# Optimization experiments

Hardware: AMD Instinct MI355X
Metric: run time of the kernel (lower is better)

## Reference

```python
import jax, jax.numpy as jnp
import numpy as np

SIZE = 128
B, S = 32, 8192


def setup_inputs() -> dict:
    key = jax.random.key(0)
    kx, = jax.random.split(key, 1)
    x = jax.random.normal(kx, (B, S, SIZE), dtype=jnp.float32)
    return {
        "x": x,
        # DyT params
        "alpha": jnp.ones((1,), jnp.float32) * 0.5,
        "dyt_weight": jnp.ones((SIZE,), jnp.float32),
        "dyt_bias": jnp.zeros((SIZE,), jnp.float32),
        # FourierForwardNetwork params
        "a_real": jnp.ones((SIZE,), jnp.float32),
        "a_imag": jnp.zeros((SIZE,), jnp.float32),
        "b_real": jnp.ones((SIZE,), jnp.float32),
        "b_imag": jnp.zeros((SIZE,), jnp.float32),
        "ffn_bias": jnp.zeros((SIZE,), jnp.float32),
    }


def reference(x, alpha, dyt_weight, dyt_bias, a_real, a_imag, b_real, b_imag, ffn_bias):
    # DyT: tanh(alpha * x) * weight + bias
    h = jnp.tanh(alpha * x) * dyt_weight + dyt_bias  # [B, S, SIZE]
    # FourierForwardNetwork. NOTE: in the original torch code the first
    # spectral branch (multiply by a, ifft, +bias, gelu) is DEAD CODE --
    # its result is overwritten by `X = torch.fft.fft(x + 0j)`. The actual
    # output is ifft(fft(h) * b).real, reproduced faithfully here.
    b = b_real + 1j * b_imag  # [SIZE] complex
    X = jnp.fft.fft(h.astype(jnp.complex64), axis=-1)  # [B, S, SIZE] complex64
    y = jnp.fft.ifft(X * b, axis=-1).real.astype(x.dtype)
    # Residual connection of FourierFFNBlock
    return y + x
```

## Files before the change

### kernel.cpp

```cpp
#include <hip/hip_runtime.h>

#define SIZE 128
#define ROWS 32
#define TPB 8
#define PITCH 136

typedef short short8 __attribute__((ext_vector_type(8)));
typedef float f32x4 __attribute__((ext_vector_type(4)));

__device__ __forceinline__ unsigned short f2bf(float f) {
    unsigned int u = __float_as_uint(f);
    unsigned int r = u + 0x7FFFu + ((u >> 16) & 1u);
    return (unsigned short)(r >> 16);
}

__global__ void build_gt(const float* __restrict__ br, const float* __restrict__ bi,
                         const float* __restrict__ w, const float* __restrict__ bias,
                         unsigned short* __restrict__ Gt, float* __restrict__ C0) {
    __shared__ float gr[SIZE];
    const int t = threadIdx.x;
    float acc = 0.0f;
    for (int j = 0; j < SIZE; ++j) {
        int p = (j * t) & 127;
        float a = (float)p * (1.0f / 64.0f);
        acc += br[j] * cospif(a) - bi[j] * sinpif(a);
    }
    gr[t] = acc * (1.0f / 128.0f);
    __syncthreads();
    float c0 = 0.0f;
    for (int k = 0; k < SIZE; ++k) {
        const float g = gr[(t - k) & 127];
        c0 += bias[k] * g;
        Gt[t * SIZE + k] = f2bf(w[k] * g);
    }
    C0[t] = c0;
}

__global__ __launch_bounds__(256, 4) void fourier_main(
    const float* __restrict__ x, const float* __restrict__ alpha_p,
    const unsigned short* __restrict__ Gt, const float* __restrict__ C0,
    float* __restrict__ out) {
    __shared__ unsigned short hA[2][ROWS * PITCH];

    const int tid = threadIdx.x;
    const int lane = tid & 63;
    const int wv = tid >> 6;
    const int lrow = lane & 15;
    const int slot = lane >> 4;
    const int colb = wv * 32;

    const float a2l = 2.0f * 1.44269504f * alpha_p[0];

    short8 gf[2][4];
    float4 c0v[2];
#pragma unroll
    for (int nt = 0; nt < 2; ++nt) {
        const int c = colb + nt * 16 + lrow;
#pragma unroll
        for (int kt = 0; kt < 4; ++kt)
            gf[nt][kt] = *reinterpret_cast<const short8*>(
                &Gt[c * SIZE + kt * 32 + slot * 8]);
        c0v[nt] = *reinterpret_cast<const float4*>(&C0[colb + nt * 16 + slot * 4]);
    }

    const unsigned blockBase = (unsigned)blockIdx.x * (TPB * ROWS * SIZE);
    const int srow = tid >> 5;
    const int scol = (tid & 31) * 4;

    auto stage = [&](int t, float4 (&xn)[4]) __attribute__((always_inline)) {
        const float* src = x + blockBase + (unsigned)t * (ROWS * SIZE);
#pragma unroll
        for (int i = 0; i < 4; ++i)
            xn[i] = *reinterpret_cast<const float4*>(&src[i * 1024 + tid * 4]);
    };
    auto hwrite = [&](int buf, const float4 (&xn)[4]) __attribute__((always_inline)) {
#pragma unroll
        for (int i = 0; i < 4; ++i) {
            ushort4 hq;
            float e;
            e = __builtin_amdgcn_exp2f(a2l * xn[i].x);
            hq.x = f2bf(fmaf(-2.0f, __builtin_amdgcn_rcpf(1.0f + e), 1.0f));
            e = __builtin_amdgcn_exp2f(a2l * xn[i].y);
            hq.y = f2bf(fmaf(-2.0f, __builtin_amdgcn_rcpf(1.0f + e), 1.0f));
            e = __builtin_amdgcn_exp2f(a2l * xn[i].z);
            hq.z = f2bf(fmaf(-2.0f, __builtin_amdgcn_rcpf(1.0f + e), 1.0f));
            e = __builtin_amdgcn_exp2f(a2l * xn[i].w);
            hq.w = f2bf(fmaf(-2.0f, __builtin_amdgcn_rcpf(1.0f + e), 1.0f));
            *reinterpret_cast<ushort4*>(&hA[buf][(i * 8 + srow) * PITCH + scol]) = hq;
        }
    };
    auto compute = [&](int t) __attribute__((always_inline)) {
        const unsigned tb = blockBase + (unsigned)t * (ROWS * SIZE);
        const unsigned short* hb = &hA[t & 1][0];
#pragma unroll
        for (int mt = 0; mt < 2; ++mt) {
            const int r = mt * 16 + lrow;
            short8 hf[4];
#pragma unroll
            for (int kt = 0; kt < 4; ++kt)
                hf[kt] = *reinterpret_cast<const short8*>(
                    &hb[r * PITCH + kt * 32 + slot * 8]);
#pragma unroll
            for (int nt = 0; nt < 2; ++nt) {
                f32x4 a = {0.f, 0.f, 0.f, 0.f};
#pragma unroll
                for (int kt = 0; kt < 4; ++kt)
                    a = __builtin_amdgcn_mfma_f32_16x16x32_bf16(gf[nt][kt], hf[kt],
                                                                a, 0, 0, 0);
                const unsigned off =
                    tb + (unsigned)r * SIZE + (unsigned)(colb + nt * 16 + slot * 4);
                const float4 xa = *reinterpret_cast<const float4*>(&x[off]);
                float4 o;
                o.x = a[0] + c0v[nt].x + xa.x;
                o.y = a[1] + c0v[nt].y + xa.y;
                o.z = a[2] + c0v[nt].z + xa.z;
                o.w = a[3] + c0v[nt].w + xa.w;
                *reinterpret_cast<float4*>(&out[off]) = o;
            }
        }
    };

    float4 xn[4];
    stage(0, xn);
    hwrite(0, xn);
    asm volatile("s_waitcnt lgkmcnt(0)\n\ts_barrier" ::: "memory");

#pragma unroll
    for (int t = 0; t < TPB; ++t) {
        if (t + 1 < TPB) stage(t + 1, xn);
        compute(t);
        if (t + 1 < TPB) {
            hwrite((t + 1) & 1, xn);
            asm volatile("s_waitcnt lgkmcnt(0)\n\ts_barrier" ::: "memory");
        }
    }
}

extern "C" void kernel_launch(void* const* d_in, const int* in_sizes, int n_in,
                              void* d_out, int out_size, void* d_ws, size_t ws_size,
                              hipStream_t stream) {
    const float* x = (const float*)d_in[0];
    const float* alpha = (const float*)d_in[1];
    const float* dyt_w = (const float*)d_in[2];
    const float* dyt_b = (const float*)d_in[3];
    const float* b_real = (const float*)d_in[6];
    const float* b_imag = (const float*)d_in[7];
    float* out = (float*)d_out;

    unsigned short* Gt = (unsigned short*)d_ws;
    float* C0 = (float*)((char*)d_ws + SIZE * SIZE * 2);

    build_gt<<<1, 128, 0, stream>>>(b_real, b_imag, dyt_w, dyt_b, Gt, C0);

    const int rows = out_size / SIZE;
    const int nblocks = rows / (ROWS * TPB);
    fourier_main<<<nblocks, 256, 0, stream>>>(x, alpha, Gt, C0, out);
}
```

Before: 76.88 us.

## Stage x in MFMA-output layout and reuse registers for residual

Each thread now loads x in the same fragment layout the MFMA output uses, so the staged float4 registers serve both the tanh/LDS write and the residual add. This removes the second global read of x per tile. It also double-buffers the register staging so loads for tile t+2 are issued while tile t computes. The cost is more live registers per thread and a less contiguous LDS write pattern, which may cause bank conflicts or reduce occupancy under the launch bounds.

```diff
diff --git a/kernel.cpp b/kernel.cpp
--- a/kernel.cpp
+++ b/kernel.cpp
@@ -64,42 +64,56 @@
     }
 
     const unsigned blockBase = (unsigned)blockIdx.x * (TPB * ROWS * SIZE);
-    const int srow = tid >> 5;
-    const int scol = (tid & 31) * 4;
+    unsigned soff[2][2];
+#pragma unroll
+    for (int mt = 0; mt < 2; ++mt)
+#pragma unroll
+        for (int nt = 0; nt < 2; ++nt)
+            soff[mt][nt] =
+                (unsigned)((mt * 16 + lrow) * SIZE + colb + nt * 16 + slot * 4);
 
-    auto stage = [&](int t, float4 (&xn)[4]) __attribute__((always_inline)) {
-        const float* src = x + blockBase + (unsigned)t * (ROWS * SIZE);
+    auto stage = [&](int t, float4 (&xs)[2][2]) __attribute__((always_inline)) {
+        const unsigned tb = blockBase + (unsigned)t * (ROWS * SIZE);
 #pragma unroll
-        for (int i = 0; i < 4; ++i)
-            xn[i] = *reinterpret_cast<const float4*>(&src[i * 1024 + tid * 4]);
+        for (int mt = 0; mt < 2; ++mt)
+#pragma unroll
+            for (int nt = 0; nt < 2; ++nt)
+                xs[mt][nt] =
+                    *reinterpret_cast<const float4*>(&x[tb + soff[mt][nt]]);
     };
-    auto hwrite = [&](int buf, const float4 (&xn)[4]) __attribute__((always_inline)) {
+    auto hwrite = [&](int buf, const float4 (&xs)[2][2])
+        __attribute__((always_inline)) {
 #pragma unroll
-        for (int i = 0; i < 4; ++i) {
-            ushort4 hq;
-            float e;
-            e = __builtin_amdgcn_exp2f(a2l * xn[i].x);
-            hq.x = f2bf(fmaf(-2.0f, __builtin_amdgcn_rcpf(1.0f + e), 1.0f));
-            e = __builtin_amdgcn_exp2f(a2l * xn[i].y);
-            hq.y = f2bf(fmaf(-2.0f, __builtin_amdgcn_rcpf(1.0f + e), 1.0f));
-            e = __builtin_amdgcn_exp2f(a2l * xn[i].z);
-            hq.z = f2bf(fmaf(-2.0f, __builtin_amdgcn_rcpf(1.0f + e), 1.0f));
-            e = __builtin_amdgcn_exp2f(a2l * xn[i].w);
-            hq.w = f2bf(fmaf(-2.0f, __builtin_amdgcn_rcpf(1.0f + e), 1.0f));
-            *reinterpret_cast<ushort4*>(&hA[buf][(i * 8 + srow) * PITCH + scol]) = hq;
-        }
+        for (int mt = 0; mt < 2; ++mt)
+#pragma unroll
+            for (int nt = 0; nt < 2; ++nt) {
+                const float4 v = xs[mt][nt];
+                ushort4 hq;
+                float e;
+                e = __builtin_amdgcn_exp2f(a2l * v.x);
+                hq.x = f2bf(fmaf(-2.0f, __builtin_amdgcn_rcpf(1.0f + e), 1.0f));
+                e = __builtin_amdgcn_exp2f(a2l * v.y);
+                hq.y = f2bf(fmaf(-2.0f, __builtin_amdgcn_rcpf(1.0f + e), 1.0f));
+                e = __builtin_amdgcn_exp2f(a2l * v.z);
+                hq.z = f2bf(fmaf(-2.0f, __builtin_amdgcn_rcpf(1.0f + e), 1.0f));
+                e = __builtin_amdgcn_exp2f(a2l * v.w);
+                hq.w = f2bf(fmaf(-2.0f, __builtin_amdgcn_rcpf(1.0f + e), 1.0f));
+                *reinterpret_cast<ushort4*>(
+                    &hA[buf][(mt * 16 + lrow) * PITCH + colb + nt * 16 +
+                             slot * 4]) = hq;
+            }
     };
-    auto compute = [&](int t) __attribute__((always_inline)) {
+    auto compute = [&](int t, const float4 (&xs)[2][2])
+        __attribute__((always_inline)) {
         const unsigned tb = blockBase + (unsigned)t * (ROWS * SIZE);
         const unsigned short* hb = &hA[t & 1][0];
 #pragma unroll
         for (int mt = 0; mt < 2; ++mt) {
-            const int r = mt * 16 + lrow;
             short8 hf[4];
 #pragma unroll
             for (int kt = 0; kt < 4; ++kt)
                 hf[kt] = *reinterpret_cast<const short8*>(
-                    &hb[r * PITCH + kt * 32 + slot * 8]);
+                    &hb[(mt * 16 + lrow) * PITCH + kt * 32 + slot * 8]);
 #pragma unroll
             for (int nt = 0; nt < 2; ++nt) {
                 f32x4 a = {0.f, 0.f, 0.f, 0.f};
@@ -107,28 +121,30 @@
                 for (int kt = 0; kt < 4; ++kt)
                     a = __builtin_amdgcn_mfma_f32_16x16x32_bf16(gf[nt][kt], hf[kt],
                                                                 a, 0, 0, 0);
-                const unsigned off =
-                    tb + (unsigned)r * SIZE + (unsigned)(colb + nt * 16 + slot * 4);
-                const float4 xa = *reinterpret_cast<const float4*>(&x[off]);
+                const float4 xa = xs[mt][nt];
                 float4 o;
                 o.x = a[0] + c0v[nt].x + xa.x;
                 o.y = a[1] + c0v[nt].y + xa.y;
                 o.z = a[2] + c0v[nt].z + xa.z;
                 o.w = a[3] + c0v[nt].w + xa.w;
-                *reinterpret_cast<float4*>(&out[off]) = o;
+                *reinterpret_cast<float4*>(&out[tb + soff[mt][nt]]) = o;
             }
         }
     };
 
-    float4 xn[4];
-    stage(0, xn);
-    hwrite(0, xn);
+    float4 xr0[2][2], xr1[2][2];
+
+    stage(0, xr0);
+    stage(1, xr1);
+    hwrite(0, xr0);
     asm volatile("s_waitcnt lgkmcnt(0)\n\ts_barrier" ::: "memory");
 
 #pragma unroll
     for (int t = 0; t < TPB; ++t) {
-        if (t + 1 < TPB) stage(t + 1, xn);
-        compute(t);
+        float4(&xc)[2][2] = (t & 1) ? xr1 : xr0;
+        float4(&xn)[2][2] = (t & 1) ? xr0 : xr1;
+        compute(t, xc);
+        if (t + 2 < TPB) stage(t + 2, xc);
         if (t + 1 < TPB) {
             hwrite((t + 1) & 1, xn);
             asm volatile("s_waitcnt lgkmcnt(0)\n\ts_barrier" ::: "memory");
```

Measured after the change: 75.12 us. -2.3%, faster.

## Stage MFMA output through LDS to reuse staged x and coalesce stores

Applied to the files above, without the earlier changes.

The MFMA results are written as bf16 into a new shared-memory output tile. A separate epilogue then reads that tile in the same row-major layout the x tile was loaded in, adds the x values already held in registers, and writes coalesced nontemporal float4 stores. This drops the second global read of x for the residual and replaces scattered fragment-layout stores. In exchange it adds a barrier per tile, doubles LDS use (which may lower occupancy), and rounds the FFT output to bf16 before the residual add, reducing accuracy.

```diff
diff --git a/kernel.cpp b/kernel.cpp
--- a/kernel.cpp
+++ b/kernel.cpp
@@ -12,6 +12,9 @@
     unsigned int u = __float_as_uint(f);
     unsigned int r = u + 0x7FFFu + ((u >> 16) & 1u);
     return (unsigned short)(r >> 16);
+}
+__device__ __forceinline__ float bf2f(unsigned short h) {
+    return __uint_as_float(((unsigned int)h) << 16);
 }
 
 __global__ void build_gt(const float* __restrict__ br, const float* __restrict__ bi,
@@ -41,6 +44,7 @@
     const unsigned short* __restrict__ Gt, const float* __restrict__ C0,
     float* __restrict__ out) {
     __shared__ unsigned short hA[2][ROWS * PITCH];
+    __shared__ unsigned short oA[2][ROWS * PITCH];
 
     const int tid = threadIdx.x;
     const int lane = tid & 63;
@@ -86,12 +90,11 @@
             hq.z = f2bf(fmaf(-2.0f, __builtin_amdgcn_rcpf(1.0f + e), 1.0f));
             e = __builtin_amdgcn_exp2f(a2l * xn[i].w);
             hq.w = f2bf(fmaf(-2.0f, __builtin_amdgcn_rcpf(1.0f + e), 1.0f));
-            *reinterpret_cast<ushort4*>(&hA[buf][(i * 8 + srow) * PITCH + scol]) = hq;
+            *reinterpret_cast<ushort4*>(&hA[buf][(i * 8 + srow) * PITCH + scol]) =
+                hq;
         }
     };
-    auto compute = [&](int t) __attribute__((always_inline)) {
-        const unsigned tb = blockBase + (unsigned)t * (ROWS * SIZE);
-        const unsigned short* hb = &hA[t & 1][0];
+    auto mfma_pass = [&](int pb) __attribute__((always_inline)) {
 #pragma unroll
         for (int mt = 0; mt < 2; ++mt) {
             const int r = mt * 16 + lrow;
@@ -99,7 +102,7 @@
 #pragma unroll
             for (int kt = 0; kt < 4; ++kt)
                 hf[kt] = *reinterpret_cast<const short8*>(
-                    &hb[r * PITCH + kt * 32 + slot * 8]);
+                    &hA[pb][r * PITCH + kt * 32 + slot * 8]);
 #pragma unroll
             for (int nt = 0; nt < 2; ++nt) {
                 f32x4 a = {0.f, 0.f, 0.f, 0.f};
@@ -107,32 +110,53 @@
                 for (int kt = 0; kt < 4; ++kt)
                     a = __builtin_amdgcn_mfma_f32_16x16x32_bf16(gf[nt][kt], hf[kt],
                                                                 a, 0, 0, 0);
-                const unsigned off =
-                    tb + (unsigned)r * SIZE + (unsigned)(colb + nt * 16 + slot * 4);
-                const float4 xa = *reinterpret_cast<const float4*>(&x[off]);
-                float4 o;
-                o.x = a[0] + c0v[nt].x + xa.x;
-                o.y = a[1] + c0v[nt].y + xa.y;
-                o.z = a[2] + c0v[nt].z + xa.z;
-                o.w = a[3] + c0v[nt].w + xa.w;
-                *reinterpret_cast<float4*>(&out[off]) = o;
+                ushort4 o;
+                o.x = f2bf(a[0] + c0v[nt].x);
+                o.y = f2bf(a[1] + c0v[nt].y);
+                o.z = f2bf(a[2] + c0v[nt].z);
+                o.w = f2bf(a[3] + c0v[nt].w);
+                *reinterpret_cast<ushort4*>(
+                    &oA[pb][r * PITCH + colb + nt * 16 + slot * 4]) = o;
             }
         }
     };
+    auto epi = [&](int t, int pb, const float4 (&xc)[4])
+        __attribute__((always_inline)) {
+        const unsigned tb = blockBase + (unsigned)t * (ROWS * SIZE);
+#pragma unroll
+        for (int i = 0; i < 4; ++i) {
+            const ushort4 ov = *reinterpret_cast<const ushort4*>(
+                &oA[pb][(i * 8 + srow) * PITCH + scol]);
+            f32x4 r;
+            r[0] = bf2f(ov.x) + xc[i].x;
+            r[1] = bf2f(ov.y) + xc[i].y;
+            r[2] = bf2f(ov.z) + xc[i].z;
+            r[3] = bf2f(ov.w) + xc[i].w;
+            __builtin_nontemporal_store(
+                r, reinterpret_cast<f32x4*>(&out[tb + i * 1024 + tid * 4]));
+        }
+    };
 
-    float4 xn[4];
-    stage(0, xn);
-    hwrite(0, xn);
+    float4 xA[4], xB[4];
+
+    stage(0, xA);
+    hwrite(0, xA);
     asm volatile("s_waitcnt lgkmcnt(0)\n\ts_barrier" ::: "memory");
 
+    auto tile_body = [&](int t, const float4 (&xc)[4], float4 (&xn)[4], int pb)
+        __attribute__((always_inline)) {
+        if (t + 1 < TPB) stage(t + 1, xn);
+        mfma_pass(pb);
+        asm volatile("s_waitcnt lgkmcnt(0)\n\ts_barrier" ::: "memory");
+        epi(t, pb, xc);
+        if (t + 1 < TPB) hwrite(pb ^ 1, xn);
+        asm volatile("s_waitcnt lgkmcnt(0)\n\ts_barrier" ::: "memory");
+    };
+
 #pragma unroll
-    for (int t = 0; t < TPB; ++t) {
-        if (t + 1 < TPB) stage(t + 1, xn);
-        compute(t);
-        if (t + 1 < TPB) {
-            hwrite((t + 1) & 1, xn);
-            asm volatile("s_waitcnt lgkmcnt(0)\n\ts_barrier" ::: "memory");
-        }
+    for (int t = 0; t < TPB; t += 2) {
+        tile_body(t, xA, xB, 0);
+        tile_body(t + 1, xB, xA, 1);
     }
 }
 
```

Measured after the change: 67.09 us. 1.15x faster.
